# Optimization experiments

Measured on AMD Instinct MI355X. Metric: run time of the kernel, lower is better.

Reference implementation:

```python
import jax, jax.numpy as jnp
import numpy as np

N_NODES = 100000
N_EDGES = 1600000


def _lin_init(k, din, dout):
    # xavier-normal-ish weight, zero bias handled separately
    s = (2.0 / (din + dout)) ** 0.5
    return jax.random.normal(k, (din, dout), jnp.float32) * s


def setup_inputs() -> dict:
    key = jax.random.key(0)
    ks = jax.random.split(key, 32)
    inp = {
        "node_feat": jax.random.normal(ks[0], (N_NODES, 3), jnp.float32),
        "edge_feat": jax.random.normal(ks[1], (N_EDGES, 1), jnp.float32),
        "edge_dist": jax.random.normal(ks[2], (N_EDGES, 1), jnp.float32),
        "src": jax.random.randint(ks[3], (N_EDGES,), 0, N_NODES),
        "dst": jax.random.randint(ks[4], (N_EDGES,), 0, N_NODES),
    }
    dims = {"enc": [3, 64, 64, 8], "dec": [8, 64, 64, 1],
            "nod": [9, 64, 64, 8], "edg": [17, 64, 64, 1]}
    i = 5
    for name, d in dims.items():
        for l in range(3):
            inp[f"w_{name}{l+1}"] = _lin_init(ks[i], d[l], d[l + 1]); i += 1
            inp[f"b_{name}{l+1}"] = jnp.zeros((d[l + 1],), jnp.float32)
    return inp


def _mlp(x, w1, b1, w2, b2, w3, b3):
    x = jax.nn.relu(x @ w1 + b1)
    x = jax.nn.relu(x @ w2 + b2)
    return jax.nn.relu(x @ w3 + b3)


def _edge_softmax(dist, dst, n):
    # softmax over incoming edges per destination node (DGL edge_softmax)
    m = jax.ops.segment_max(dist, dst, num_segments=n)          # [N,1]
    e = jnp.exp(dist - m[dst])                                   # [E,1]
    s = jax.ops.segment_sum(e, dst, num_segments=n)              # [N,1]
    return e / s[dst]


def reference(node_feat, edge_feat, edge_dist, src, dst,
              w_enc1, b_enc1, w_enc2, b_enc2, w_enc3, b_enc3,
              w_dec1, b_dec1, w_dec2, b_dec2, w_dec3, b_dec3,
              w_nod1, b_nod1, w_nod2, b_nod2, w_nod3, b_nod3,
              w_edg1, b_edg1, w_edg2, b_edg2, w_edg3, b_edg3):
    n = node_feat.shape[0]
    # encoder: [N,3] -> [N,8]
    h = _mlp(node_feat, w_enc1, b_enc1, w_enc2, b_enc2, w_enc3, b_enc3)
    # softmax-weighted aggregation of src features to dst
    w = _edge_softmax(edge_dist, dst, n)                         # [E,1]
    h = jax.ops.segment_sum(w * h[src], dst, num_segments=n)     # [N,8]
    he = edge_feat                                               # [E,1]
    for _ in range(2):
        x = jnp.concatenate([he, h[src], h[dst]], axis=-1)       # [E,17]
        he = _mlp(x, w_edg1, b_edg1, w_edg2, b_edg2, w_edg3, b_edg3)  # [E,1]
        agg = jax.ops.segment_sum(he, dst, num_segments=n)       # [N,1]
        h = _mlp(jnp.concatenate([agg, h], axis=-1),
                 w_nod1, b_nod1, w_nod2, b_nod2, w_nod3, b_nod3)  # [N,8]
    # second softmax aggregation (same dist -> same weights)
    h = jax.ops.segment_sum(w * h[src], dst, num_segments=n)     # [N,8]
    # decoder: [N,8] -> [N,1]
    return _mlp(h, w_dec1, b_dec1, w_dec2, b_dec2, w_dec3, b_dec3)
```

## Files before the change

### kernel.cpp

```cpp
#include <hip/hip_runtime.h>

#define N_NODES 100000
#define N_EDGES 1600000


__global__ void zero_kernel(float* p, int n) {
    int i = blockIdx.x * blockDim.x + threadIdx.x;
    int stride = gridDim.x * blockDim.x;
    for (; i < n; i += stride) p[i] = 0.f;
}

__global__ void exp_sum_kernel(const float* __restrict__ dist, const int* __restrict__ dst,
                               float* __restrict__ s, float* __restrict__ wbuf, int E) {
    int e = blockIdx.x * blockDim.x + threadIdx.x;
    if (e >= E) return;
    float v = expf(dist[e]);
    wbuf[e] = v;
    atomicAdd(s + dst[e], v);
}

template <bool NORM>
__global__ void agg_kernel(float* wbuf, const float* __restrict__ s,
                           const float* __restrict__ hfeat,
                           const int* __restrict__ src, const int* __restrict__ dst,
                           float* __restrict__ out, int E) {
    int t = blockIdx.x * blockDim.x + threadIdx.x;
    if (t >= E * 8) return;
    int e = t >> 3, c = t & 7;
    float w = wbuf[e];
    int d = dst[e];
    if (NORM) {
        w = w / s[d];
        if (c == 0) wbuf[e] = w;
    }
    atomicAdd(out + d * 8 + c, w * hfeat[src[e] * 8 + c]);
}

struct PackArgs { const float *w1, *b1, *w2; float* out; int din, stride; };

__global__ void pack_kernel(PackArgs a0, PackArgs a1, PackArgs a2, PackArgs a3) {
    PackArgs a = (blockIdx.x == 0) ? a0 : (blockIdx.x == 1) ? a1
               : (blockIdx.x == 2) ? a2 : a3;
    int k = threadIdx.x;
    float* row = a.out + k * a.stride;
    for (int j = 0; j < 64; ++j) row[j] = a.w2[k * 64 + j];
    for (int j = 0; j < a.din; ++j) row[64 + j] = a.w1[j * 64 + k];
    row[64 + a.din] = a.b1[k];
}

template <int DIN, int DOUT, int STRIDE>
__device__ __forceinline__ void mlp_fused(
    const float* __restrict__ x, const float* __restrict__ wp,
    const float* __restrict__ b2,
    const float* __restrict__ w3, const float* __restrict__ b3,
    float* __restrict__ out) {
    float h2[64];
#pragma unroll
    for (int j = 0; j < 64; ++j) h2[j] = b2[j];
    for (int k = 0; k < 64; ++k) {
        const float* row = wp + k * STRIDE;
        float a = row[64 + DIN];
#pragma unroll
        for (int j = 0; j < DIN; ++j) a = fmaf(x[j], row[64 + j], a);
        a = fmaxf(a, 0.f);
#pragma unroll
        for (int j = 0; j < 64; ++j) h2[j] = fmaf(a, row[j], h2[j]);
    }
    float acc[DOUT];
#pragma unroll
    for (int o = 0; o < DOUT; ++o) acc[o] = b3[o];
#pragma unroll
    for (int j = 0; j < 64; ++j) {
        float r = fmaxf(h2[j], 0.f);
#pragma unroll
        for (int o = 0; o < DOUT; ++o) acc[o] = fmaf(r, w3[j * DOUT + o], acc[o]);
    }
#pragma unroll
    for (int o = 0; o < DOUT; ++o) out[o] = fmaxf(acc[o], 0.f);
}

template <int CA, int CB, int DOUT, int STRIDE>
__global__ __launch_bounds__(256, 3) void node_mlp_kernel(
    const float* __restrict__ xa, const float* __restrict__ xb,
    const float* __restrict__ wp, const float* __restrict__ b2,
    const float* __restrict__ w3, const float* __restrict__ b3,
    float* __restrict__ out, int n) {
    constexpr int DIN = CA + CB;
    int i = blockIdx.x * 256 + threadIdx.x;
    if (i >= n) return;
    float x[DIN];
#pragma unroll
    for (int k = 0; k < CA; ++k) x[k] = xa[i * CA + k];
    if (CB == 8) {
        float4 v0 = *(const float4*)(xb + i * 8);
        float4 v1 = *(const float4*)(xb + i * 8 + 4);
        x[CA + 0] = v0.x; x[CA + 1] = v0.y; x[CA + 2] = v0.z; x[CA + 3] = v0.w;
        x[CA + 4] = v1.x; x[CA + 5] = v1.y; x[CA + 6] = v1.z; x[CA + 7] = v1.w;
    }
    float o[DOUT];
    mlp_fused<DIN, DOUT, STRIDE>(x, wp, b2, w3, b3, o);
#pragma unroll
    for (int k = 0; k < DOUT; ++k) out[i * DOUT + k] = o[k];
}

__global__ __launch_bounds__(256, 3) void edge_mlp_kernel(
    const float* __restrict__ he_in, const float* __restrict__ h,
    const int* __restrict__ src, const int* __restrict__ dst,
    const float* __restrict__ wp, const float* __restrict__ b2,
    const float* __restrict__ w3, const float* __restrict__ b3,
    float* __restrict__ he_out, float* __restrict__ agg, int E) {
    int e = blockIdx.x * 256 + threadIdx.x;
    if (e >= E) return;
    int d = dst[e], sr = src[e];
    float x[17];
    x[0] = he_in[e];
    float4 a0 = *(const float4*)(h + sr * 8);
    float4 a1 = *(const float4*)(h + sr * 8 + 4);
    float4 d0 = *(const float4*)(h + d * 8);
    float4 d1 = *(const float4*)(h + d * 8 + 4);
    x[1] = a0.x;  x[2] = a0.y;  x[3] = a0.z;  x[4] = a0.w;
    x[5] = a1.x;  x[6] = a1.y;  x[7] = a1.z;  x[8] = a1.w;
    x[9] = d0.x;  x[10] = d0.y; x[11] = d0.z; x[12] = d0.w;
    x[13] = d1.x; x[14] = d1.y; x[15] = d1.z; x[16] = d1.w;
    float o;
    mlp_fused<17, 1, 96>(x, wp, b2, w3, b3, &o);
    he_out[e] = o;
    atomicAdd(agg + d, o);
}

extern "C" void kernel_launch(void* const* d_in, const int* in_sizes, int n_in,
                              void* d_out, int out_size, void* d_ws, size_t ws_size,
                              hipStream_t stream) {
    const int N = N_NODES, E = N_EDGES;
    const float* node_feat = (const float*)d_in[0];
    const float* edge_feat = (const float*)d_in[1];
    const float* edge_dist = (const float*)d_in[2];
    const int* src = (const int*)d_in[3];
    const int* dst = (const int*)d_in[4];
    const float* w_enc1 = (const float*)d_in[5];  const float* b_enc1 = (const float*)d_in[6];
    const float* w_enc2 = (const float*)d_in[7];  const float* b_enc2 = (const float*)d_in[8];
    const float* w_enc3 = (const float*)d_in[9];  const float* b_enc3 = (const float*)d_in[10];
    const float* w_dec1 = (const float*)d_in[11]; const float* b_dec1 = (const float*)d_in[12];
    const float* w_dec2 = (const float*)d_in[13]; const float* b_dec2 = (const float*)d_in[14];
    const float* w_dec3 = (const float*)d_in[15]; const float* b_dec3 = (const float*)d_in[16];
    const float* w_nod1 = (const float*)d_in[17]; const float* b_nod1 = (const float*)d_in[18];
    const float* w_nod2 = (const float*)d_in[19]; const float* b_nod2 = (const float*)d_in[20];
    const float* w_nod3 = (const float*)d_in[21]; const float* b_nod3 = (const float*)d_in[22];
    const float* w_edg1 = (const float*)d_in[23]; const float* b_edg1 = (const float*)d_in[24];
    const float* w_edg2 = (const float*)d_in[25]; const float* b_edg2 = (const float*)d_in[26];
    const float* w_edg3 = (const float*)d_in[27]; const float* b_edg3 = (const float*)d_in[28];

    float* ws = (float*)d_ws;
    float* s      = ws;
    float* hagg1  = ws + N;
    float* agg1   = ws + 9 * N;
    float* agg2   = ws + 10 * N;
    float* hagg2  = ws + 11 * N;
    float* h_enc  = ws + 19 * N;
    float* h_r1   = ws + 27 * N;
    float* h_r2   = ws + 35 * N;
    float* wbuf   = ws + 43 * N;
    float* he1    = wbuf + E;
    float* he2    = he1 + E;
    float* pk_enc = he2 + E;
    float* pk_nod = pk_enc + 64 * 80;
    float* pk_edg = pk_nod + 64 * 80;
    float* pk_dec = pk_edg + 64 * 96;

    PackArgs pa0{w_enc1, b_enc1, w_enc2, pk_enc, 3, 80};
    PackArgs pa1{w_nod1, b_nod1, w_nod2, pk_nod, 9, 80};
    PackArgs pa2{w_edg1, b_edg1, w_edg2, pk_edg, 17, 96};
    PackArgs pa3{w_dec1, b_dec1, w_dec2, pk_dec, 8, 80};
    pack_kernel<<<4, 64, 0, stream>>>(pa0, pa1, pa2, pa3);

    zero_kernel<<<2048, 256, 0, stream>>>(ws, 19 * N);
    node_mlp_kernel<3, 0, 8, 80><<<(N + 255) / 256, 256, 0, stream>>>(node_feat, nullptr,
        pk_enc, b_enc2, w_enc3, b_enc3, h_enc, N);
    exp_sum_kernel<<<(E + 255) / 256, 256, 0, stream>>>(edge_dist, dst, s, wbuf, E);
    agg_kernel<true><<<(E * 8 + 255) / 256, 256, 0, stream>>>(wbuf, s, h_enc, src, dst, hagg1, E);
    edge_mlp_kernel<<<(E + 255) / 256, 256, 0, stream>>>(edge_feat, hagg1, src, dst,
        pk_edg, b_edg2, w_edg3, b_edg3, he1, agg1, E);
    node_mlp_kernel<1, 8, 8, 80><<<(N + 255) / 256, 256, 0, stream>>>(agg1, hagg1,
        pk_nod, b_nod2, w_nod3, b_nod3, h_r1, N);
    edge_mlp_kernel<<<(E + 255) / 256, 256, 0, stream>>>(he1, h_r1, src, dst,
        pk_edg, b_edg2, w_edg3, b_edg3, he2, agg2, E);
    node_mlp_kernel<1, 8, 8, 80><<<(N + 255) / 256, 256, 0, stream>>>(agg2, h_r1,
        pk_nod, b_nod2, w_nod3, b_nod3, h_r2, N);
    agg_kernel<false><<<(E * 8 + 255) / 256, 256, 0, stream>>>(wbuf, s, h_r2, src, dst, hagg2, E);
    node_mlp_kernel<8, 0, 1, 80><<<(N + 255) / 256, 256, 0, stream>>>(hagg2, nullptr,
        pk_dec, b_dec2, w_dec3, b_dec3, (float*)d_out, N);
}
```

Baseline: 827.8 us.

## Run edge MLP on MFMA with split-bf16 hi/lo emulation of fp32

Replaces the per-thread scalar FP32 edge MLP with a wave-level matrix-core kernel. Each wave handles 64 edges: it gathers the 17 input features, splits each value into bf16 hi and lo parts, and runs layers 1 and 2 with three bf16 MFMAs per tile (hi*hi, hi*lo, lo*hi) to approximate FP32 accuracy. A new pack kernel pre-splits the edge weights into hi/lo bf16. Layer 3 is a shuffle reduction across lanes. The aim is to remove the ALU-bound FMA cost of the dominant edge MLP, at the cost of a small precision loss and the assumption that E is a multiple of 128.

```diff
diff --git a/kernel.cpp b/kernel.cpp
--- a/kernel.cpp
+++ b/kernel.cpp
@@ -3,6 +3,17 @@
 #define N_NODES 100000
 #define N_EDGES 1600000
 
+typedef __attribute__((ext_vector_type(4))) float f32x4;
+typedef __attribute__((ext_vector_type(8))) short bf16x8;
+
+__device__ __forceinline__ unsigned short f2bf(float v) {
+    unsigned u = __float_as_uint(v);
+    unsigned r = (u + 0x7FFFu + ((u >> 16) & 1u)) >> 16;
+    return (unsigned short)r;
+}
+__device__ __forceinline__ float bf2f(unsigned short h) {
+    return __uint_as_float(((unsigned)h) << 16);
+}
 
 __global__ void zero_kernel(float* p, int n) {
     int i = blockIdx.x * blockDim.x + threadIdx.x;
@@ -38,14 +49,31 @@
 
 struct PackArgs { const float *w1, *b1, *w2; float* out; int din, stride; };
 
-__global__ void pack_kernel(PackArgs a0, PackArgs a1, PackArgs a2, PackArgs a3) {
-    PackArgs a = (blockIdx.x == 0) ? a0 : (blockIdx.x == 1) ? a1
-               : (blockIdx.x == 2) ? a2 : a3;
+__global__ void pack_kernel(PackArgs a0, PackArgs a1, PackArgs a2) {
+    PackArgs a = (blockIdx.x == 0) ? a0 : (blockIdx.x == 1) ? a1 : a2;
     int k = threadIdx.x;
     float* row = a.out + k * a.stride;
     for (int j = 0; j < 64; ++j) row[j] = a.w2[k * 64 + j];
     for (int j = 0; j < a.din; ++j) row[64 + j] = a.w1[j * 64 + k];
     row[64 + a.din] = a.b1[k];
+}
+
+__global__ void pack_edge_kernel(const float* __restrict__ w1, const float* __restrict__ w2,
+                                 unsigned short* __restrict__ w1hi, unsigned short* __restrict__ w1lo,
+                                 unsigned short* __restrict__ w2hi, unsigned short* __restrict__ w2lo) {
+    int c = threadIdx.x;
+    for (int j = 0; j < 32; ++j) {
+        float v = (j < 17) ? w1[j * 64 + c] : 0.f;
+        unsigned short hi = f2bf(v);
+        w1hi[c * 32 + j] = hi;
+        w1lo[c * 32 + j] = f2bf(v - bf2f(hi));
+    }
+    for (int k = 0; k < 64; ++k) {
+        float v = w2[k * 64 + c];
+        unsigned short hi = f2bf(v);
+        w2hi[c * 64 + k] = hi;
+        w2lo[c * 64 + k] = f2bf(v - bf2f(hi));
+    }
 }
 
 template <int DIN, int DOUT, int STRIDE>
@@ -103,29 +131,163 @@
     for (int k = 0; k < DOUT; ++k) out[i * DOUT + k] = o[k];
 }
 
-__global__ __launch_bounds__(256, 3) void edge_mlp_kernel(
+__global__ __launch_bounds__(128, 2) void edge_mlp_mfma_kernel(
     const float* __restrict__ he_in, const float* __restrict__ h,
     const int* __restrict__ src, const int* __restrict__ dst,
-    const float* __restrict__ wp, const float* __restrict__ b2,
+    const unsigned short* __restrict__ w1hi, const unsigned short* __restrict__ w1lo,
+    const unsigned short* __restrict__ w2hi, const unsigned short* __restrict__ w2lo,
+    const float* __restrict__ b1, const float* __restrict__ b2,
     const float* __restrict__ w3, const float* __restrict__ b3,
-    float* __restrict__ he_out, float* __restrict__ agg, int E) {
-    int e = blockIdx.x * 256 + threadIdx.x;
-    if (e >= E) return;
-    int d = dst[e], sr = src[e];
-    float x[17];
-    x[0] = he_in[e];
-    float4 a0 = *(const float4*)(h + sr * 8);
-    float4 a1 = *(const float4*)(h + sr * 8 + 4);
-    float4 d0 = *(const float4*)(h + d * 8);
-    float4 d1 = *(const float4*)(h + d * 8 + 4);
-    x[1] = a0.x;  x[2] = a0.y;  x[3] = a0.z;  x[4] = a0.w;
-    x[5] = a1.x;  x[6] = a1.y;  x[7] = a1.z;  x[8] = a1.w;
-    x[9] = d0.x;  x[10] = d0.y; x[11] = d0.z; x[12] = d0.w;
-    x[13] = d1.x; x[14] = d1.y; x[15] = d1.z; x[16] = d1.w;
-    float o;
-    mlp_fused<17, 1, 96>(x, wp, b2, w3, b3, &o);
-    he_out[e] = o;
-    atomicAdd(agg + d, o);
+    float* __restrict__ he_out, float* __restrict__ agg) {
+    __shared__ __align__(16) unsigned char smem[2 * 18432];
+    const int lane = threadIdx.x & 63, wv = threadIdx.x >> 6;
+    unsigned char* W = smem + wv * 18432;
+    const int ebase = (blockIdx.x * 2 + wv) * 64;
+
+    {
+        int e = ebase + lane;
+        float x[32];
+        x[0] = he_in[e];
+        int sr = src[e], dd = dst[e];
+        float4 a0 = *(const float4*)(h + sr * 8);
+        float4 a1 = *(const float4*)(h + sr * 8 + 4);
+        float4 d0 = *(const float4*)(h + dd * 8);
+        float4 d1 = *(const float4*)(h + dd * 8 + 4);
+        x[1] = a0.x;  x[2] = a0.y;  x[3] = a0.z;  x[4] = a0.w;
+        x[5] = a1.x;  x[6] = a1.y;  x[7] = a1.z;  x[8] = a1.w;
+        x[9] = d0.x;  x[10] = d0.y; x[11] = d0.z; x[12] = d0.w;
+        x[13] = d1.x; x[14] = d1.y; x[15] = d1.z; x[16] = d1.w;
+#pragma unroll
+        for (int j = 17; j < 32; ++j) x[j] = 0.f;
+        unsigned uh[16], ul[16];
+#pragma unroll
+        for (int jj = 0; jj < 16; ++jj) {
+            unsigned short h0 = f2bf(x[2 * jj]);
+            unsigned short h1v = f2bf(x[2 * jj + 1]);
+            unsigned short l0 = f2bf(x[2 * jj] - bf2f(h0));
+            unsigned short l1 = f2bf(x[2 * jj + 1] - bf2f(h1v));
+            uh[jj] = (unsigned)h0 | ((unsigned)h1v << 16);
+            ul[jj] = (unsigned)l0 | ((unsigned)l1 << 16);
+        }
+        uint4* ph = (uint4*)(W + lane * 80);
+        uint4* pl = (uint4*)(W + 5120 + lane * 80);
+#pragma unroll
+        for (int q = 0; q < 4; ++q) {
+            ph[q] = make_uint4(uh[4 * q], uh[4 * q + 1], uh[4 * q + 2], uh[4 * q + 3]);
+            pl[q] = make_uint4(ul[4 * q], ul[4 * q + 1], ul[4 * q + 2], ul[4 * q + 3]);
+        }
+    }
+    __syncthreads();
+    const int row = lane & 15, g = lane >> 4;
+
+    bf16x8 wa_h[4], wa_l[4];
+#pragma unroll
+    for (int mt = 0; mt < 4; ++mt) {
+        wa_h[mt] = *(const bf16x8*)(w1hi + (16 * mt + row) * 32 + g * 8);
+        wa_l[mt] = *(const bf16x8*)(w1lo + (16 * mt + row) * 32 + g * 8);
+    }
+    bf16x8 xb_h[4], xb_l[4];
+#pragma unroll
+    for (int nt = 0; nt < 4; ++nt) {
+        xb_h[nt] = *(const bf16x8*)(W + (16 * nt + row) * 80 + g * 16);
+        xb_l[nt] = *(const bf16x8*)(W + 5120 + (16 * nt + row) * 80 + g * 16);
+    }
+    f32x4 c1[4][4];
+#pragma unroll
+    for (int mt = 0; mt < 4; ++mt)
+#pragma unroll
+        for (int nt = 0; nt < 4; ++nt) {
+            f32x4 c = {0.f, 0.f, 0.f, 0.f};
+            c = __builtin_amdgcn_mfma_f32_16x16x32_bf16(wa_h[mt], xb_h[nt], c, 0, 0, 0);
+            c = __builtin_amdgcn_mfma_f32_16x16x32_bf16(wa_h[mt], xb_l[nt], c, 0, 0, 0);
+            c = __builtin_amdgcn_mfma_f32_16x16x32_bf16(wa_l[mt], xb_h[nt], c, 0, 0, 0);
+            c1[mt][nt] = c;
+        }
+    float4 b1v[4];
+#pragma unroll
+    for (int mt = 0; mt < 4; ++mt) b1v[mt] = *(const float4*)(b1 + 16 * mt + g * 4);
+#pragma unroll
+    for (int mt = 0; mt < 4; ++mt)
+#pragma unroll
+        for (int nt = 0; nt < 4; ++nt) {
+            int el = 16 * nt + row;
+            int ch0 = 16 * mt + g * 4;
+            float v0 = fmaxf(c1[mt][nt].x + b1v[mt].x, 0.f);
+            float v1 = fmaxf(c1[mt][nt].y + b1v[mt].y, 0.f);
+            float v2 = fmaxf(c1[mt][nt].z + b1v[mt].z, 0.f);
+            float v3 = fmaxf(c1[mt][nt].w + b1v[mt].w, 0.f);
+            unsigned short h0 = f2bf(v0), h1v = f2bf(v1), h2v = f2bf(v2), h3 = f2bf(v3);
+            unsigned hh0 = (unsigned)h0 | ((unsigned)h1v << 16);
+            unsigned hh1 = (unsigned)h2v | ((unsigned)h3 << 16);
+            unsigned ll0 = (unsigned)f2bf(v0 - bf2f(h0)) | ((unsigned)f2bf(v1 - bf2f(h1v)) << 16);
+            unsigned ll1 = (unsigned)f2bf(v2 - bf2f(h2v)) | ((unsigned)f2bf(v3 - bf2f(h3)) << 16);
+            *(uint2*)(W + el * 144 + ch0 * 2) = make_uint2(hh0, hh1);
+            *(uint2*)(W + 9216 + el * 144 + ch0 * 2) = make_uint2(ll0, ll1);
+        }
+    __syncthreads();
+
+    bf16x8 w2a_h[4][2], w2a_l[4][2];
+#pragma unroll
+    for (int mt = 0; mt < 4; ++mt)
+#pragma unroll
+        for (int ks = 0; ks < 2; ++ks) {
+            w2a_h[mt][ks] = *(const bf16x8*)(w2hi + (16 * mt + row) * 64 + ks * 32 + g * 8);
+            w2a_l[mt][ks] = *(const bf16x8*)(w2lo + (16 * mt + row) * 64 + ks * 32 + g * 8);
+        }
+    f32x4 c2[4][4];
+#pragma unroll
+    for (int mt = 0; mt < 4; ++mt)
+#pragma unroll
+        for (int nt = 0; nt < 4; ++nt) c2[mt][nt] = (f32x4){0.f, 0.f, 0.f, 0.f};
+#pragma unroll
+    for (int nt = 0; nt < 4; ++nt) {
+        bf16x8 hb_h[2], hb_l[2];
+#pragma unroll
+        for (int ks = 0; ks < 2; ++ks) {
+            hb_h[ks] = *(const bf16x8*)(W + (16 * nt + row) * 144 + (ks * 32 + g * 8) * 2);
+            hb_l[ks] = *(const bf16x8*)(W + 9216 + (16 * nt + row) * 144 + (ks * 32 + g * 8) * 2);
+        }
+#pragma unroll
+        for (int mt = 0; mt < 4; ++mt)
+#pragma unroll
+            for (int ks = 0; ks < 2; ++ks) {
+                c2[mt][nt] = __builtin_amdgcn_mfma_f32_16x16x32_bf16(w2a_h[mt][ks], hb_h[ks], c2[mt][nt], 0, 0, 0);
+                c2[mt][nt] = __builtin_amdgcn_mfma_f32_16x16x32_bf16(w2a_h[mt][ks], hb_l[ks], c2[mt][nt], 0, 0, 0);
+                c2[mt][nt] = __builtin_amdgcn_mfma_f32_16x16x32_bf16(w2a_l[mt][ks], hb_h[ks], c2[mt][nt], 0, 0, 0);
+            }
+    }
+
+    float4 b2v[4], w3v[4];
+#pragma unroll
+    for (int mt = 0; mt < 4; ++mt) {
+        b2v[mt] = *(const float4*)(b2 + 16 * mt + g * 4);
+        w3v[mt] = *(const float4*)(w3 + 16 * mt + g * 4);
+    }
+    float b3s = b3[0];
+    float pacc[4];
+#pragma unroll
+    for (int nt = 0; nt < 4; ++nt) {
+        float p = 0.f;
+#pragma unroll
+        for (int mt = 0; mt < 4; ++mt) {
+            p = fmaf(fmaxf(c2[mt][nt].x + b2v[mt].x, 0.f), w3v[mt].x, p);
+            p = fmaf(fmaxf(c2[mt][nt].y + b2v[mt].y, 0.f), w3v[mt].y, p);
+            p = fmaf(fmaxf(c2[mt][nt].z + b2v[mt].z, 0.f), w3v[mt].z, p);
+            p = fmaf(fmaxf(c2[mt][nt].w + b2v[mt].w, 0.f), w3v[mt].w, p);
+        }
+        p += __shfl_xor(p, 16);
+        p += __shfl_xor(p, 32);
+        pacc[nt] = p;
+    }
+    if (lane < 16) {
+#pragma unroll
+        for (int nt = 0; nt < 4; ++nt) {
+            int e2 = ebase + 16 * nt + lane;
+            float o = fmaxf(pacc[nt] + b3s, 0.f);
+            he_out[e2] = o;
+            atomicAdd(agg + dst[e2], o);
+        }
+    }
 }
 
 extern "C" void kernel_launch(void* const* d_in, const int* in_sizes, int n_in,
@@ -164,26 +326,29 @@
     float* he2    = he1 + E;
     float* pk_enc = he2 + E;
     float* pk_nod = pk_enc + 64 * 80;
-    float* pk_edg = pk_nod + 64 * 80;
-    float* pk_dec = pk_edg + 64 * 96;
+    float* pk_dec = pk_nod + 64 * 80;
+    unsigned short* w1hi = (unsigned short*)(pk_dec + 64 * 80);
+    unsigned short* w1lo = w1hi + 64 * 32;
+    unsigned short* w2hi = w1lo + 64 * 32;
+    unsigned short* w2lo = w2hi + 64 * 64;
 
     PackArgs pa0{w_enc1, b_enc1, w_enc2, pk_enc, 3, 80};
     PackArgs pa1{w_nod1, b_nod1, w_nod2, pk_nod, 9, 80};
-    PackArgs pa2{w_edg1, b_edg1, w_edg2, pk_edg, 17, 96};
-    PackArgs pa3{w_dec1, b_dec1, w_dec2, pk_dec, 8, 80};
-    pack_kernel<<<4, 64, 0, stream>>>(pa0, pa1, pa2, pa3);
+    PackArgs pa2{w_dec1, b_dec1, w_dec2, pk_dec, 8, 80};
+    pack_kernel<<<3, 64, 0, stream>>>(pa0, pa1, pa2);
+    pack_edge_kernel<<<1, 64, 0, stream>>>(w_edg1, w_edg2, w1hi, w1lo, w2hi, w2lo);
 
     zero_kernel<<<2048, 256, 0, stream>>>(ws, 19 * N);
     node_mlp_kernel<3, 0, 8, 80><<<(N + 255) / 256, 256, 0, stream>>>(node_feat, nullptr,
         pk_enc, b_enc2, w_enc3, b_enc3, h_enc, N);
     exp_sum_kernel<<<(E + 255) / 256, 256, 0, stream>>>(edge_dist, dst, s, wbuf, E);
     agg_kernel<true><<<(E * 8 + 255) / 256, 256, 0, stream>>>(wbuf, s, h_enc, src, dst, hagg1, E);
-    edge_mlp_kernel<<<(E + 255) / 256, 256, 0, stream>>>(edge_feat, hagg1, src, dst,
-        pk_edg, b_edg2, w_edg3, b_edg3, he1, agg1, E);
+    edge_mlp_mfma_kernel<<<E / 128, 128, 0, stream>>>(edge_feat, hagg1, src, dst,
+        w1hi, w1lo, w2hi, w2lo, b_edg1, b_edg2, w_edg3, b_edg3, he1, agg1);
     node_mlp_kernel<1, 8, 8, 80><<<(N + 255) / 256, 256, 0, stream>>>(agg1, hagg1,
         pk_nod, b_nod2, w_nod3, b_nod3, h_r1, N);
-    edge_mlp_kernel<<<(E + 255) / 256, 256, 0, stream>>>(he1, h_r1, src, dst,
-        pk_edg, b_edg2, w_edg3, b_edg3, he2, agg2, E);
+    edge_mlp_mfma_kernel<<<E / 128, 128, 0, stream>>>(he1, h_r1, src, dst,
+        w1hi, w1lo, w2hi, w2lo, b_edg1, b_edg2, w_edg3, b_edg3, he2, agg2);
     node_mlp_kernel<1, 8, 8, 80><<<(N + 255) / 256, 256, 0, stream>>>(agg2, h_r1,
         pk_nod, b_nod2, w_nod3, b_nod3, h_r2, N);
     agg_kernel<false><<<(E * 8 + 255) / 256, 256, 0, stream>>>(wbuf, s, h_r2, src, dst, hagg2, E);
```

Result: faster. 798.4 us (-3.5%).
